# Kernel optimization log

Hardware: AMD Instinct MI355X
Metric: run time of the kernel (lower is better)

The kernel has to match this reference:

```python
import jax, jax.numpy as jnp
import numpy as np

N_ROIS, ROI_DIM, D, H, L, FF, NCLS = 200, 199, 192, 6, 3, 576, 2
EPS = 1e-5

def _ln(x, g, b):
    m = jnp.mean(x, axis=-1, keepdims=True)
    v = jnp.mean((x - m) ** 2, axis=-1, keepdims=True)
    return (x - m) * jax.lax.rsqrt(v + EPS) * g + b

def _gelu(x):
    return jax.nn.gelu(x, approximate=False)

def _mha(q, k, v, Wqkv, bqkv, Wo, bo):
    # q: [B,Q,D], k/v: [B,S,D]; Wqkv: [3,D,D], bqkv: [3,D]
    B, Q, _ = q.shape
    S = k.shape[1]
    Dh = D // H
    qp = (q @ Wqkv[0] + bqkv[0]).reshape(B, Q, H, Dh)
    kp = (k @ Wqkv[1] + bqkv[1]).reshape(B, S, H, Dh)
    vp = (v @ Wqkv[2] + bqkv[2]).reshape(B, S, H, Dh)
    scores = jnp.einsum('bqhd,bkhd->bhqk', qp, kp) / jnp.sqrt(jnp.float32(Dh))
    attn = jax.nn.softmax(scores, axis=-1)
    out = jnp.einsum('bhqk,bkhd->bqhd', attn, vp).reshape(B, Q, D)
    return out @ Wo + bo

def setup_inputs() -> dict:
    key = jax.random.key(0)
    ks = iter(jax.random.split(key, 40))
    r = lambda *s: jax.random.normal(next(ks), s, dtype=jnp.float32) * 0.02
    inp = {
        'x': jax.random.normal(next(ks), (256, N_ROIS * ROI_DIM), dtype=jnp.float32),
        # 200 distinct per-ROI tokenizers, stacked for a single batched GEMM
        'roi_W': r(N_ROIS, ROI_DIM, D), 'roi_b': r(N_ROIS, D),
        'roi_ln_g': jnp.ones((N_ROIS, D), jnp.float32), 'roi_ln_b': jnp.zeros((N_ROIS, D), jnp.float32),
        'pos_emb': r(N_ROIS, D),
        # encoder layers stacked on leading L dim
        'enc_Wqkv': r(L, 3, D, D), 'enc_bqkv': r(L, 3, D),
        'enc_Wo': r(L, D, D), 'enc_bo': r(L, D),
        'enc_ln1_g': jnp.ones((L, D), jnp.float32), 'enc_ln1_b': jnp.zeros((L, D), jnp.float32),
        'enc_W1': r(L, D, FF), 'enc_b1': r(L, FF),
        'enc_W2': r(L, FF, D), 'enc_b2': r(L, D),
        'enc_ln2_g': jnp.ones((L, D), jnp.float32), 'enc_ln2_b': jnp.zeros((L, D), jnp.float32),
        # attention pooling MHA
        'pool_Wqkv': r(3, D, D), 'pool_bqkv': r(3, D),
        'pool_Wo': r(D, D), 'pool_bo': r(D),
        # classifier head
        'cls_ln_g': jnp.ones((D,), jnp.float32), 'cls_ln_b': jnp.zeros((D,), jnp.float32),
        'cls_W1': r(D, D // 2), 'cls_b1': r(D // 2),
        'cls_W2': r(D // 2, D // 4), 'cls_b2': r(D // 4),
        'cls_W3': r(D // 4, NCLS), 'cls_b3': r(NCLS),
    }
    return inp

def reference(x, roi_W, roi_b, roi_ln_g, roi_ln_b, pos_emb,
              enc_Wqkv, enc_bqkv, enc_Wo, enc_bo, enc_ln1_g, enc_ln1_b,
              enc_W1, enc_b1, enc_W2, enc_b2, enc_ln2_g, enc_ln2_b,
              pool_Wqkv, pool_bqkv, pool_Wo, pool_bo,
              cls_ln_g, cls_ln_b, cls_W1, cls_b1, cls_W2, cls_b2, cls_W3, cls_b3):
    B = x.shape[0]
    roi = x.reshape(B, N_ROIS, ROI_DIM)
    # fused per-ROI Linear (200 distinct weights) as one batched GEMM
    tok = jnp.einsum('brf,rfd->brd', roi, roi_W) + roi_b  # [B,200,192]
    tok = _gelu(_ln(tok, roi_ln_g, roi_ln_b))  # dropout = identity (eval)
    tok = tok + pos_emb[None]
    # post-norm transformer encoder (PyTorch default norm_first=False)
    h = tok
    for i in range(L):
        a = _mha(h, h, h, enc_Wqkv[i], enc_bqkv[i], enc_Wo[i], enc_bo[i])
        h = _ln(h + a, enc_ln1_g[i], enc_ln1_b[i])
        f = _gelu(h @ enc_W1[i] + enc_b1[i]) @ enc_W2[i] + enc_b2[i]
        h = _ln(h + f, enc_ln2_g[i], enc_ln2_b[i])
    # MHA pooling: query = mean over ROI tokens
    q = jnp.mean(h, axis=1, keepdims=True)  # [B,1,D]
    pooled = _mha(q, h, h, pool_Wqkv, pool_bqkv, pool_Wo, pool_bo)[:, 0]  # [B,D]
    # classifier
    z = _ln(pooled, cls_ln_g, cls_ln_b)
    z = _gelu(z @ cls_W1 + cls_b1)
    z = _gelu(z @ cls_W2 + cls_b2)
    return z @ cls_W3 + cls_b3
```

## Files before the change

### kernel.cpp

```cpp
#include <hip/hip_runtime.h>
#include <math.h>


typedef unsigned short u16;
typedef unsigned int u32;
typedef __attribute__((ext_vector_type(8))) __bf16 bf16x8;
typedef __attribute__((ext_vector_type(4))) float f32x4;

#define GLL16(gp, lp) __builtin_amdgcn_global_load_lds(                 \
    (const __attribute__((address_space(1))) void*)(gp),                \
    (__attribute__((address_space(3))) void*)(lp), 16, 0, 0)

#define FENCE_VM()   do { asm volatile("s_waitcnt vmcnt(0)" ::: "memory");  \
                          __builtin_amdgcn_sched_barrier(0); } while (0)
#define FENCE_LGKM() do { asm volatile("s_waitcnt lgkmcnt(0)" ::: "memory");\
                          __builtin_amdgcn_sched_barrier(0); } while (0)

__device__ __forceinline__ u16 f2bf(float x) {
    u32 u = __float_as_uint(x);
    u = (u + 0x7FFFu + ((u >> 16) & 1u)) >> 16;
    return (u16)u;
}
__device__ __forceinline__ float bf2f(u16 h) {
    return __uint_as_float(((u32)h) << 16);
}

__device__ __forceinline__ float gelu_exact(float x) {
    return 0.5f * x * (1.0f + erff(x * 0.7071067811865475f));
}

__device__ __forceinline__ float wave_sum(float v) {
#pragma unroll
    for (int o = 32; o > 0; o >>= 1) v += __shfl_xor(v, o, 64);
    return v;
}
__device__ __forceinline__ float wave_max(float v) {
#pragma unroll
    for (int o = 32; o > 0; o >>= 1) v = fmaxf(v, __shfl_xor(v, o, 64));
    return v;
}
__device__ __forceinline__ float row_sum16(float v) {
    v += __shfl_xor(v, 1, 64); v += __shfl_xor(v, 2, 64);
    v += __shfl_xor(v, 4, 64); v += __shfl_xor(v, 8, 64);
    return v;
}

__device__ __forceinline__ f32x4 mfma_bf16(bf16x8 a, bf16x8 b, f32x4 c) {
    return __builtin_amdgcn_mfma_f32_16x16x32_bf16(a, b, c, 0, 0, 0);
}

__global__ void conv_wt(const float* __restrict__ W, u16* __restrict__ oh,
                        int K, int N)
{
    const long z = blockIdx.z;
    const int idx = blockIdx.x * 256 + threadIdx.x;
    if (idx >= K * N) return;
    const int k = idx / N, n = idx - k * N;
    const float x = W[z * K * N + idx];
    oh[z * (long)K * N + (long)n * K + k] = f2bf(x);
}

__global__ void conv_x(const float* __restrict__ x, u16* __restrict__ xh)
{
    const long idx = (long)blockIdx.x * 256 + threadIdx.x;
    if (idx >= 200L * 256 * 224) return;
    const int k = (int)(idx % 224);
    const long t = idx / 224;
    const int m = (int)(t % 256);
    const int z = (int)(t / 256);
    const float v = (k < 199) ? x[(long)m * 39800 + z * 199 + k] : 0.f;
    xh[idx] = f2bf(v);
}

__global__ void conv_roiw(const float* __restrict__ W, u16* __restrict__ oh)
{
    __shared__ float tile[32][33];
    const int z = blockIdx.z;
    const int k0 = blockIdx.x * 32;
    const int n0 = blockIdx.y * 32;
    for (int i = threadIdx.y; i < 32; i += 8) {
        const int k = k0 + i, n = n0 + threadIdx.x;
        tile[i][threadIdx.x] = (k < 199) ? W[((long)z * 199 + k) * 192 + n] : 0.f;
    }
    __syncthreads();
    for (int i = threadIdx.y; i < 32; i += 8) {
        const int n = n0 + i, k = k0 + threadIdx.x;
        const float v = tile[threadIdx.x][i];
        oh[((long)z * 192 + n) * 224 + k] = f2bf(v);
    }
}

template<int EPI>
__global__ __launch_bounds__(256, 3) void gemm_mfma(
    const u16* __restrict__ Ah,
    const u16* __restrict__ Bh,
    const float* __restrict__ bias,
    float* __restrict__ C, u16* __restrict__ Ch,
    u16* __restrict__ Hh, u16* __restrict__ Hl,
    const float* __restrict__ lng, const float* __restrict__ lnb,
    int N, int K)
{
    __shared__ u16 Ash[128][32];
    __shared__ u16 Bsh[192][32];

    const int tid = threadIdx.x;
    const int wave = tid >> 6, lane = tid & 63;
    const int lm = lane & 15, quad = lane >> 4;
    const long m0 = (long)blockIdx.x * 128;
    const int n0 = blockIdx.y * 192;
    const int lrow = lane >> 2;
    const int lch  = (((lane & 3) ^ (lrow & 3)) * 8);
    const int sq   = (quad ^ (lm & 3)) * 8;

    const u16* pA0h = Ah + (m0 + wave * 32 +  0 + lrow) * K + lch;
    const u16* pA1h = Ah + (m0 + wave * 32 + 16 + lrow) * K + lch;
    const u16* pB0h = Bh + (long)(n0 + wave * 48 +  0 + lrow) * K + lch;
    const u16* pB1h = Bh + (long)(n0 + wave * 48 + 16 + lrow) * K + lch;
    const u16* pB2h = Bh + (long)(n0 + wave * 48 + 32 + lrow) * K + lch;

    auto stage = [&](int k0) {
        GLL16(pA0h + k0, &Ash[wave * 32][0]);
        GLL16(pA1h + k0, &Ash[wave * 32 + 16][0]);
        GLL16(pB0h + k0, &Bsh[wave * 48][0]);
        GLL16(pB1h + k0, &Bsh[wave * 48 + 16][0]);
        GLL16(pB2h + k0, &Bsh[wave * 48 + 32][0]);
    };

    f32x4 acc[2][12];
#pragma unroll
    for (int i = 0; i < 2; i++)
#pragma unroll
        for (int j = 0; j < 12; j++)
#pragma unroll
            for (int r = 0; r < 4; r++) acc[i][j][r] = 0.f;

    const int kt = K >> 5;
    stage(0);
    FENCE_VM();
    __syncthreads();

    for (int t = 0; t < kt; t++) {
        bf16x8 afh[2];
#pragma unroll
        for (int mi = 0; mi < 2; mi++)
            afh[mi] = *(const bf16x8*)&Ash[wave * 32 + mi * 16 + lm][sq];
#pragma unroll
        for (int g = 0; g < 4; g++) {
            bf16x8 bfh[3];
#pragma unroll
            for (int j = 0; j < 3; j++)
                bfh[j] = *(const bf16x8*)&Bsh[g * 48 + j * 16 + lm][sq];
#pragma unroll
            for (int mi = 0; mi < 2; mi++)
#pragma unroll
                for (int j = 0; j < 3; j++) {
                    const int ni = g * 3 + j;
                    acc[mi][ni] = mfma_bf16(afh[mi], bfh[j], acc[mi][ni]);
                }
        }
        if (t + 1 < kt) {
            __syncthreads();
            stage((t + 1) << 5);
            FENCE_VM();
            __syncthreads();
        }
    }

    if (EPI == 5) {
        float gv[12], bv2[12], biasv[12];
#pragma unroll
        for (int ni = 0; ni < 12; ni++) {
            const int col = ni * 16 + lm;
            gv[ni] = lng[col]; bv2[ni] = lnb[col]; biasv[ni] = bias[col];
        }
#pragma unroll
        for (int mi = 0; mi < 2; mi++) {
#pragma unroll
            for (int r = 0; r < 4; r++) {
                const long row = m0 + wave * 32 + mi * 16 + quad * 4 + r;
                const long rb = row * 192;
                float vals[12];
                float s = 0.f;
#pragma unroll
                for (int ni = 0; ni < 12; ni++) {
                    const int col = ni * 16 + lm;
                    const float hval = bf2f(Hh[rb + col]) + bf2f(Hl[rb + col]);
                    vals[ni] = acc[mi][ni][r] + biasv[ni] + hval;
                    s += vals[ni];
                }
                const float mean = row_sum16(s) * (1.f / 192.f);
                float ss = 0.f;
#pragma unroll
                for (int ni = 0; ni < 12; ni++) {
                    vals[ni] -= mean;
                    ss += vals[ni] * vals[ni];
                }
                const float var = row_sum16(ss) * (1.f / 192.f);
                const float rsr = 1.f / sqrtf(var + 1e-5f);
#pragma unroll
                for (int ni = 0; ni < 12; ni++) {
                    const int col = ni * 16 + lm;
                    const float y = vals[ni] * rsr * gv[ni] + bv2[ni];
                    const u16 hb = f2bf(y);
                    Hh[rb + col] = hb;
                    Hl[rb + col] = f2bf(y - bf2f(hb));
                }
            }
        }
        return;
    }

#pragma unroll
    for (int mi = 0; mi < 2; mi++) {
        const long rowb = m0 + wave * 32 + mi * 16 + quad * 4;
#pragma unroll
        for (int ni = 0; ni < 12; ni++) {
            const int col = n0 + ni * 16 + lm;
            const float bv = bias[col];
#pragma unroll
            for (int r = 0; r < 4; r++) {
                float v = acc[mi][ni][r] + bv;
                if (EPI == 0) {
                    C[(rowb + r) * N + col] = v;
                } else {
                    if (EPI == 2) v = gelu_exact(v);
                    Ch[(rowb + r) * N + col] = f2bf(v);
                }
            }
        }
    }
}

__global__ __launch_bounds__(256, 3) void tok_mfma(
    const u16* __restrict__ xh,
    const u16* __restrict__ wth,
    const float* __restrict__ roi_b,
    const float* __restrict__ lng, const float* __restrict__ lnb,
    const float* __restrict__ pos,
    u16* __restrict__ hh, u16* __restrict__ hl)
{
    __shared__ u16 Ash[128][32];
    __shared__ u16 Bsh[192][32];

    const int tid = threadIdx.x;
    const int wave = tid >> 6, lane = tid & 63;
    const int lm = lane & 15, quad = lane >> 4;
    const int m0 = blockIdx.x * 128;
    const int z = blockIdx.y;
    const int lrow = lane >> 2;
    const int lch  = (((lane & 3) ^ (lrow & 3)) * 8);
    const int sq   = (quad ^ (lm & 3)) * 8;
    const int K = 224;

    const u16* pA0h = xh + ((long)z * 256 + m0 + wave * 32 +  0 + lrow) * K + lch;
    const u16* pA1h = xh + ((long)z * 256 + m0 + wave * 32 + 16 + lrow) * K + lch;
    const u16* pB0h = wth + ((long)z * 192 + wave * 48 +  0 + lrow) * K + lch;
    const u16* pB1h = wth + ((long)z * 192 + wave * 48 + 16 + lrow) * K + lch;
    const u16* pB2h = wth + ((long)z * 192 + wave * 48 + 32 + lrow) * K + lch;

    auto stage = [&](int k0) {
        GLL16(pA0h + k0, &Ash[wave * 32][0]);
        GLL16(pA1h + k0, &Ash[wave * 32 + 16][0]);
        GLL16(pB0h + k0, &Bsh[wave * 48][0]);
        GLL16(pB1h + k0, &Bsh[wave * 48 + 16][0]);
        GLL16(pB2h + k0, &Bsh[wave * 48 + 32][0]);
    };

    f32x4 acc[2][12];
#pragma unroll
    for (int i = 0; i < 2; i++)
#pragma unroll
        for (int j = 0; j < 12; j++)
#pragma unroll
            for (int r = 0; r < 4; r++) acc[i][j][r] = 0.f;

    stage(0);
    FENCE_VM();
    __syncthreads();
    for (int t = 0; t < 7; t++) {
        bf16x8 afh[2];
#pragma unroll
        for (int mi = 0; mi < 2; mi++)
            afh[mi] = *(const bf16x8*)&Ash[wave * 32 + mi * 16 + lm][sq];
#pragma unroll
        for (int g = 0; g < 4; g++) {
            bf16x8 bfh[3];
#pragma unroll
            for (int j = 0; j < 3; j++)
                bfh[j] = *(const bf16x8*)&Bsh[g * 48 + j * 16 + lm][sq];
#pragma unroll
            for (int mi = 0; mi < 2; mi++)
#pragma unroll
                for (int j = 0; j < 3; j++) {
                    const int ni = g * 3 + j;
                    acc[mi][ni] = mfma_bf16(afh[mi], bfh[j], acc[mi][ni]);
                }
        }
        if (t + 1 < 7) {
            __syncthreads();
            stage((t + 1) << 5);
            FENCE_VM();
            __syncthreads();
        }
    }

    float gv[12], bv2[12], biasv[12], pv[12];
#pragma unroll
    for (int ni = 0; ni < 12; ni++) {
        const int col = ni * 16 + lm;
        gv[ni]    = lng[z * 192 + col];
        bv2[ni]   = lnb[z * 192 + col];
        biasv[ni] = roi_b[z * 192 + col];
        pv[ni]    = pos[z * 192 + col];
    }
#pragma unroll
    for (int mi = 0; mi < 2; mi++) {
#pragma unroll
        for (int r = 0; r < 4; r++) {
            const int brow = m0 + wave * 32 + mi * 16 + quad * 4 + r;
            float vals[12];
            float s = 0.f;
#pragma unroll
            for (int ni = 0; ni < 12; ni++) {
                vals[ni] = acc[mi][ni][r] + biasv[ni];
                s += vals[ni];
            }
            const float mean = row_sum16(s) * (1.f / 192.f);
            float ss = 0.f;
#pragma unroll
            for (int ni = 0; ni < 12; ni++) {
                vals[ni] -= mean;
                ss += vals[ni] * vals[ni];
            }
            const float var = row_sum16(ss) * (1.f / 192.f);
            const float rsr = 1.f / sqrtf(var + 1e-5f);
            const long ob = ((long)brow * 200 + z) * 192;
#pragma unroll
            for (int ni = 0; ni < 12; ni++) {
                const int col = ni * 16 + lm;
                const float y = gelu_exact(vals[ni] * rsr * gv[ni] + bv2[ni]) + pv[ni];
                const u16 hb = f2bf(y);
                hh[ob + col] = hb;
                hl[ob + col] = f2bf(y - bf2f(hb));
            }
        }
    }
}

template<int EPI>
__global__ __launch_bounds__(256) void gemm_kernel(
    const float* __restrict__ A, int lda, long strideA,
    const float* __restrict__ Bw, long strideB,
    const float* __restrict__ bias, long strideBias,
    float* __restrict__ C, int ldc, long strideC,
    int M, int N, int K, int ldb)
{
    __shared__ float As[16][132];
    __shared__ float Bs[16][68];

    const int z = blockIdx.z;
    const float* Ab    = A    + (long)z * strideA;
    const float* Bb    = Bw   + (long)z * strideB;
    const float* biasb = bias + (long)z * strideBias;
    float*       Cb    = C    + (long)z * strideC;

    const int row0 = blockIdx.x * 128;
    const int col0 = blockIdx.y * 64;
    const int tid  = threadIdx.x;
    const int tm = tid >> 4;
    const int tn = tid & 15;

    const int la_m = tid >> 1;
    const int la_k = (tid & 1) * 8;
    const int lb_k = tid >> 4;
    const int lb_n = (tid & 15) * 4;

    const float* bcol = Bb + (col0 + lb_n);
    const float* arow = Ab + (long)(row0 + la_m) * lda;
    const bool vecA = ((lda & 3) == 0) &&
                      ((((unsigned long long)(const void*)arow) & 15ull) == 0ull);

    float acc[8][4];
#pragma unroll
    for (int i = 0; i < 8; i++)
#pragma unroll
        for (int j = 0; j < 4; j++) acc[i][j] = 0.f;

    for (int k0 = 0; k0 < K; k0 += 16) {
        if (vecA && (k0 + 16 <= K)) {
            float4 v0 = *(const float4*)(arow + k0 + la_k);
            float4 v1 = *(const float4*)(arow + k0 + la_k + 4);
            As[la_k + 0][la_m] = v0.x; As[la_k + 1][la_m] = v0.y;
            As[la_k + 2][la_m] = v0.z; As[la_k + 3][la_m] = v0.w;
            As[la_k + 4][la_m] = v1.x; As[la_k + 5][la_m] = v1.y;
            As[la_k + 6][la_m] = v1.z; As[la_k + 7][la_m] = v1.w;
        } else {
#pragma unroll
            for (int i = 0; i < 8; i++) {
                int k = k0 + la_k + i;
                As[la_k + i][la_m] = (k < K) ? arow[k] : 0.f;
            }
        }
        {
            int k = k0 + lb_k;
            float4 v = make_float4(0.f, 0.f, 0.f, 0.f);
            if (k < K) v = *(const float4*)(bcol + (long)k * ldb);
            *(float4*)&Bs[lb_k][lb_n] = v;
        }
        __syncthreads();
#pragma unroll
        for (int kk = 0; kk < 16; kk++) {
            float4 a0 = *(const float4*)&As[kk][tm * 8];
            float4 a1 = *(const float4*)&As[kk][tm * 8 + 4];
            float4 b4 = *(const float4*)&Bs[kk][tn * 4];
            float av[8] = {a0.x, a0.y, a0.z, a0.w, a1.x, a1.y, a1.z, a1.w};
            float bv[4] = {b4.x, b4.y, b4.z, b4.w};
#pragma unroll
            for (int i = 0; i < 8; i++)
#pragma unroll
                for (int j = 0; j < 4; j++) acc[i][j] += av[i] * bv[j];
        }
        __syncthreads();
    }

    const int gcol = col0 + tn * 4;
    float4 bv4 = *(const float4*)(biasb + gcol);
#pragma unroll
    for (int i = 0; i < 8; i++) {
        int grow = row0 + tm * 8 + i;
        float4 o;
        o.x = acc[i][0] + bv4.x; o.y = acc[i][1] + bv4.y;
        o.z = acc[i][2] + bv4.z; o.w = acc[i][3] + bv4.w;
        if (EPI == 1) {
            o.x = gelu_exact(o.x); o.y = gelu_exact(o.y);
            o.z = gelu_exact(o.z); o.w = gelu_exact(o.w);
        }
        *(float4*)(Cb + (long)grow * ldc + gcol) = o;
    }
}

__global__ __launch_bounds__(256, 2) void attn_enc_mfma(
    const u16* __restrict__ qkvh, u16* __restrict__ outh)
{
    __shared__ u16 Ksh[96][40];
    __shared__ u16 Vth[32][104];
    __shared__ u16 Pbuf[4][16][40];

    const int bh = blockIdx.x;
    const int b = bh / 6, h = bh % 6;
    const int tid = threadIdx.x;
    const int wave = tid >> 6, lane = tid & 63;
    const int lm = lane & 15, quad = lane >> 4;
    const int nq = (wave == 0) ? 4 : 3;

    uint4 qh[4];
#pragma unroll
    for (int i = 0; i < 4; i++) {
        if (i < nq) {
            int qt = wave + 4 * i;
            int qrow = qt * 16 + lm; if (qrow > 199) qrow = 199;
            const long off = (long)(b * 200 + qrow) * 576 + h * 32 + quad * 8;
            qh[i] = *(const uint4*)(qkvh + off);
        }
    }

    float mrow[4][4], lrow[4][4];
    f32x4 accO[4][2];
#pragma unroll
    for (int i = 0; i < 4; i++)
#pragma unroll
        for (int r = 0; r < 4; r++) {
            mrow[i][r] = -1e30f; lrow[i][r] = 0.f;
            accO[i][0][r] = 0.f; accO[i][1][r] = 0.f;
        }

    const float scale = 0.17677669529663688f;

#pragma unroll
    for (int ph = 0; ph < 3; ph++) {
        const int base = (ph == 0) ? 0 : (ph == 1) ? 96 : 192;
        const int ntl  = (ph == 2) ? 2 : 6;
        const int nslot = ntl * 16;

        __syncthreads();
        if (wave < 2) {
            const int sub = wave * 64 + lane;
#pragma unroll
            for (int rep = 0; rep < 3; rep++) {
                const int idx = rep * 128 + sub;
                if (idx < nslot * 4) {
                    const int key = idx >> 2, ch = idx & 3;
                    const int gk = base + key;
                    const bool valid = gk < 200;
                    const long roff = (long)(b * 200 + (valid ? gk : 0)) * 576
                                      + h * 32 + 192 + ch * 8;
                    uint4 v = valid ? *(const uint4*)(qkvh + roff)
                                    : make_uint4(0, 0, 0, 0);
                    *(uint4*)(&Ksh[0][0] + key * 40 + ch * 8) = v;
                }
            }
        } else {
            const int sub = (wave - 2) * 64 + lane;
#pragma unroll
            for (int rep = 0; rep < 2; rep++) {
                const int idx = rep * 128 + sub;
                if (idx < nslot * 2) {
                    const int key = idx >> 1, hf = idx & 1;
                    const int gk = base + key;
                    const bool valid = gk < 200;
                    const long roff = (long)(b * 200 + (valid ? gk : 0)) * 576
                                      + h * 32 + 384 + hf * 16;
                    uint4 v0 = valid ? *(const uint4*)(qkvh + roff)
                                     : make_uint4(0, 0, 0, 0);
                    uint4 v1 = valid ? *(const uint4*)(qkvh + roff + 8)
                                     : make_uint4(0, 0, 0, 0);
                    const u16* p0 = (const u16*)&v0;
                    const u16* p1 = (const u16*)&v1;
#pragma unroll
                    for (int j = 0; j < 8; j++) {
                        Vth[hf * 16 + j][key]     = p0[j];
                        Vth[hf * 16 + 8 + j][key] = p1[j];
                    }
                }
            }
        }
        __syncthreads();

#pragma unroll
        for (int i = 0; i < 4; i++) {
            if (i >= nq) continue;
            const bf16x8 qhf = *(const bf16x8*)&qh[i];
            float s[6][4];
#pragma unroll
            for (int ni = 0; ni < 6; ni++) {
                if (ni >= ntl) continue;
                bf16x8 kh8 = *(const bf16x8*)&Ksh[ni * 16 + lm][quad * 8];
                f32x4 c = {0.f, 0.f, 0.f, 0.f};
                c = mfma_bf16(qhf, kh8, c);
                const bool masked = (base + ni * 16 + lm) >= 200;
#pragma unroll
                for (int r = 0; r < 4; r++)
                    s[ni][r] = masked ? -1e30f : c[r] * scale;
            }
            float fac[4];
#pragma unroll
            for (int r = 0; r < 4; r++) {
                float pm = s[0][r];
#pragma unroll
                for (int ni = 1; ni < 6; ni++)
                    if (ni < ntl) pm = fmaxf(pm, s[ni][r]);
                pm = fmaxf(pm, __shfl_xor(pm, 1, 64));
                pm = fmaxf(pm, __shfl_xor(pm, 2, 64));
                pm = fmaxf(pm, __shfl_xor(pm, 4, 64));
                pm = fmaxf(pm, __shfl_xor(pm, 8, 64));
                const float mn = fmaxf(mrow[i][r], pm);
                fac[r] = __expf(mrow[i][r] - mn);
                mrow[i][r] = mn;
                float ps = 0.f;
#pragma unroll
                for (int ni = 0; ni < 6; ni++) {
                    if (ni >= ntl) continue;
                    float e = __expf(s[ni][r] - mn);
                    s[ni][r] = e;
                    ps += e;
                }
                ps += __shfl_xor(ps, 1, 64);
                ps += __shfl_xor(ps, 2, 64);
                ps += __shfl_xor(ps, 4, 64);
                ps += __shfl_xor(ps, 8, 64);
                lrow[i][r] = lrow[i][r] * fac[r] + ps;
                accO[i][0][r] *= fac[r];
                accO[i][1][r] *= fac[r];
            }
#pragma unroll
            for (int ck = 0; ck < 3; ck++) {
                if (ck >= (ntl >> 1)) continue;
                FENCE_LGKM();
#pragma unroll
                for (int tl = 0; tl < 2; tl++) {
#pragma unroll
                    for (int r = 0; r < 4; r++) {
                        Pbuf[wave][quad * 4 + r][tl * 16 + lm] =
                            f2bf(s[2 * ck + tl][r]);
                    }
                }
                FENCE_LGKM();
                const bf16x8 pa = *(const bf16x8*)&Pbuf[wave][lm][quad * 8];
#pragma unroll
                for (int nt = 0; nt < 2; nt++) {
                    bf16x8 vh8 = *(const bf16x8*)&Vth[nt * 16 + lm][ck * 32 + quad * 8];
                    accO[i][nt] = mfma_bf16(pa, vh8, accO[i][nt]);
                }
            }
        }
    }

#pragma unroll
    for (int i = 0; i < 4; i++) {
        if (i >= nq) continue;
        const int qt = wave + 4 * i;
#pragma unroll
        for (int r = 0; r < 4; r++) {
            const int qrow = qt * 16 + quad * 4 + r;
            if (qrow >= 200) continue;
            const float inv = 1.f / lrow[i][r];
            const long ob = (long)(b * 200 + qrow) * 192 + h * 32 + lm;
            outh[ob]      = f2bf(accO[i][0][r] * inv);
            outh[ob + 16] = f2bf(accO[i][1][r] * inv);
        }
    }
}

__global__ __launch_bounds__(192) void mean_tokens_pair(
    const u16* __restrict__ hh, const u16* __restrict__ hl, float* __restrict__ qmean)
{
    const int b = blockIdx.x, d = threadIdx.x;
    float s = 0.f;
    for (int r = 0; r < 200; r++) {
        const long idx = ((long)b * 200 + r) * 192 + d;
        s += bf2f(hh[idx]) + bf2f(hl[idx]);
    }
    qmean[b * 192 + d] = s * (1.f / 200.f);
}

__global__ __launch_bounds__(64) void attn_pool(
    const float* __restrict__ qp, const float* __restrict__ kv,
    float* __restrict__ out)
{
    __shared__ float p[200];
    const int b = blockIdx.x / 6, h = blockIdx.x % 6;
    const int lane = threadIdx.x;

    const float* qrow = qp + b * 192 + h * 32;
    float qr[32];
#pragma unroll
    for (int u = 0; u < 8; u++) {
        float4 t = *(const float4*)(qrow + 4 * u);
        qr[4 * u] = t.x; qr[4 * u + 1] = t.y;
        qr[4 * u + 2] = t.z; qr[4 * u + 3] = t.w;
    }
    const float scale = 0.17677669529663688f;
    const float* kb = kv + (long)(b * 200) * 384 + h * 32;
    float s[4];
    float mymax = -1e30f;
#pragma unroll
    for (int g = 0; g < 4; g++) {
        int j = lane + 64 * g;
        if (j < 200) {
            const float* kr = kb + (long)j * 384;
            float acc = 0.f;
#pragma unroll
            for (int u = 0; u < 8; u++) {
                float4 k4 = *(const float4*)(kr + 4 * u);
                acc += qr[4 * u] * k4.x + qr[4 * u + 1] * k4.y +
                       qr[4 * u + 2] * k4.z + qr[4 * u + 3] * k4.w;
            }
            s[g] = acc * scale;
            mymax = fmaxf(mymax, s[g]);
        } else {
            s[g] = -1e30f;
        }
    }
    float mx = wave_max(mymax);
    float psum = 0.f;
#pragma unroll
    for (int g = 0; g < 4; g++) {
        int j = lane + 64 * g;
        if (j < 200) {
            float e = __expf(s[g] - mx);
            p[j] = e;
            psum += e;
        }
    }
    float tot = wave_sum(psum);
    __syncthreads();
    const int half = lane >> 5, d = lane & 31;
    const float* vb = kv + (long)(b * 200) * 384 + 192 + h * 32 + d;
    float acc = 0.f;
    for (int jj = 0; jj < 100; jj++) {
        int j = half * 100 + jj;
        acc += p[j] * vb[(long)j * 384];
    }
    acc += __shfl_xor(acc, 32, 64);
    acc /= tot;
    if (lane < 32) out[b * 192 + h * 32 + d] = acc;
}

__global__ __launch_bounds__(64) void classifier_kernel(
    const float* __restrict__ pooled,
    const float* __restrict__ g, const float* __restrict__ bt,
    const float* __restrict__ W1, const float* __restrict__ b1,
    const float* __restrict__ W2, const float* __restrict__ b2,
    const float* __restrict__ W3, const float* __restrict__ b3,
    float* __restrict__ out)
{
    __shared__ float z[192];
    __shared__ float z1[96];
    __shared__ float z2[48];
    const int b = blockIdx.x, lane = threadIdx.x;
    const float* pr = pooled + b * 192;
    float x0 = pr[lane], x1 = pr[lane + 64], x2 = pr[lane + 128];
    float m = wave_sum(x0 + x1 + x2) * (1.f / 192.f);
    float d0 = x0 - m, d1 = x1 - m, d2 = x2 - m;
    float v = wave_sum(d0 * d0 + d1 * d1 + d2 * d2) * (1.f / 192.f);
    float rs = 1.f / sqrtf(v + 1e-5f);
    z[lane]       = d0 * rs * g[lane]       + bt[lane];
    z[lane + 64]  = d1 * rs * g[lane + 64]  + bt[lane + 64];
    z[lane + 128] = d2 * rs * g[lane + 128] + bt[lane + 128];
    __syncthreads();
#pragma unroll
    for (int rep = 0; rep < 2; rep++) {
        int j = lane + rep * 64;
        if (j < 96) {
            float a = b1[j];
            for (int k = 0; k < 192; k++) a += z[k] * W1[k * 96 + j];
            z1[j] = gelu_exact(a);
        }
    }
    __syncthreads();
    if (lane < 48) {
        float a = b2[lane];
        for (int k = 0; k < 96; k++) a += z1[k] * W2[k * 48 + lane];
        z2[lane] = gelu_exact(a);
    }
    __syncthreads();
    if (lane < 2) {
        float a = b3[lane];
        for (int k = 0; k < 48; k++) a += z2[k] * W3[k * 2 + lane];
        out[b * 2 + lane] = a;
    }
}

extern "C" void kernel_launch(void* const* d_in, const int* in_sizes, int n_in,
                              void* d_out, int out_size, void* d_ws, size_t ws_size,
                              hipStream_t stream)
{
    (void)in_sizes; (void)n_in; (void)out_size; (void)ws_size;

    const float* x         = (const float*)d_in[0];
    const float* roi_W     = (const float*)d_in[1];
    const float* roi_b     = (const float*)d_in[2];
    const float* roi_ln_g  = (const float*)d_in[3];
    const float* roi_ln_b  = (const float*)d_in[4];
    const float* pos_emb   = (const float*)d_in[5];
    const float* enc_Wqkv  = (const float*)d_in[6];
    const float* enc_bqkv  = (const float*)d_in[7];
    const float* enc_Wo    = (const float*)d_in[8];
    const float* enc_bo    = (const float*)d_in[9];
    const float* enc_ln1_g = (const float*)d_in[10];
    const float* enc_ln1_b = (const float*)d_in[11];
    const float* enc_W1    = (const float*)d_in[12];
    const float* enc_b1    = (const float*)d_in[13];
    const float* enc_W2    = (const float*)d_in[14];
    const float* enc_b2    = (const float*)d_in[15];
    const float* enc_ln2_g = (const float*)d_in[16];
    const float* enc_ln2_b = (const float*)d_in[17];
    const float* pool_Wqkv = (const float*)d_in[18];
    const float* pool_bqkv = (const float*)d_in[19];
    const float* pool_Wo   = (const float*)d_in[20];
    const float* pool_bo   = (const float*)d_in[21];
    const float* cls_ln_g  = (const float*)d_in[22];
    const float* cls_ln_b  = (const float*)d_in[23];
    const float* cls_W1    = (const float*)d_in[24];
    const float* cls_b1    = (const float*)d_in[25];
    const float* cls_W2    = (const float*)d_in[26];
    const float* cls_b2    = (const float*)d_in[27];
    const float* cls_W3    = (const float*)d_in[28];
    const float* cls_b3    = (const float*)d_in[29];

    char* ws = (char*)d_ws;
    u16*   hh    = (u16*)(ws);
    u16*   hl    = (u16*)(ws + 19660800);
    char*  bufA  = ws + 39321600;
    float* bufAf = (float*)bufA;
    u16*   xh    = (u16*)bufA;
    u16*   wth   = (u16*)(bufA + 45875200);
    u16*   qkvh  = (u16*)bufA;
    u16*   ffh   = (u16*)bufA;
    char*  bufB  = ws + 157286400;
    u16*   bBh   = (u16*)bufB;
    float* qmean = (float*)(ws + 196608000);
    float* qp    = qmean + 49152;
    float* pattn = qp + 49152;
    float* pooled= pattn + 49152;
    char*  wts   = ws + 197394432;
    u16* WqkvH = (u16*)(wts);
    u16* Wff1H = (u16*)(wts + 1327104);
    u16* Wff2H = (u16*)(wts + 2654208);
    u16* WwoH  = (u16*)(wts + 3981312);
    u16* WkvH  = (u16*)(wts + 4423680);

    conv_wt<<<dim3(144, 1, 9), 256, 0, stream>>>(enc_Wqkv, WqkvH, 192, 192);
    conv_wt<<<dim3(432, 1, 3), 256, 0, stream>>>(enc_W1, Wff1H, 192, 576);
    conv_wt<<<dim3(432, 1, 3), 256, 0, stream>>>(enc_W2, Wff2H, 576, 192);
    conv_wt<<<dim3(144, 1, 3), 256, 0, stream>>>(enc_Wo, WwoH, 192, 192);
    conv_wt<<<dim3(144, 1, 2), 256, 0, stream>>>(pool_Wqkv + 36864, WkvH, 192, 192);

    conv_x<<<44800, 256, 0, stream>>>(x, xh);
    conv_roiw<<<dim3(7, 6, 200), dim3(32, 8), 0, stream>>>(roi_W, wth);
    tok_mfma<<<dim3(2, 200), 256, 0, stream>>>(
        xh, wth, roi_b, roi_ln_g, roi_ln_b, pos_emb, hh, hl);

    for (int i = 0; i < 3; i++) {
        gemm_mfma<3><<<dim3(400, 3), 256, 0, stream>>>(
            hh, WqkvH + (long)i * 110592,
            enc_bqkv + i * 576, nullptr, qkvh,
            nullptr, nullptr, nullptr, nullptr, 576, 192);
        attn_enc_mfma<<<1536, 256, 0, stream>>>(qkvh, bBh);
        gemm_mfma<5><<<dim3(400, 1), 256, 0, stream>>>(
            bBh, WwoH + (long)i * 36864,
            enc_bo + i * 192, nullptr, nullptr,
            hh, hl, enc_ln1_g + i * 192, enc_ln1_b + i * 192, 192, 192);
        gemm_mfma<2><<<dim3(400, 3), 256, 0, stream>>>(
            hh, Wff1H + (long)i * 110592,
            enc_b1 + i * 576, nullptr, ffh,
            nullptr, nullptr, nullptr, nullptr, 576, 192);
        gemm_mfma<5><<<dim3(400, 1), 256, 0, stream>>>(
            ffh, Wff2H + (long)i * 110592,
            enc_b2 + i * 192, nullptr, nullptr,
            hh, hl, enc_ln2_g + i * 192, enc_ln2_b + i * 192, 192, 576);
    }

    mean_tokens_pair<<<256, 192, 0, stream>>>(hh, hl, qmean);
    gemm_kernel<0><<<dim3(2, 3, 1), 256, 0, stream>>>(
        qmean, 192, 0, pool_Wqkv, 0, pool_bqkv, 0, qp, 192, 0, 256, 192, 192, 192);
    gemm_mfma<0><<<dim3(400, 2), 256, 0, stream>>>(
        hh, WkvH, pool_bqkv + 192,
        bufAf, nullptr,
        nullptr, nullptr, nullptr, nullptr, 384, 192);
    attn_pool<<<1536, 64, 0, stream>>>(qp, bufAf, pattn);
    gemm_kernel<0><<<dim3(2, 3, 1), 256, 0, stream>>>(
        pattn, 192, 0, pool_Wo, 0, pool_bo, 0, pooled, 192, 0, 256, 192, 192, 192);

    classifier_kernel<<<256, 64, 0, stream>>>(
        pooled, cls_ln_g, cls_ln_b,
        cls_W1, cls_b1, cls_W2, cls_b2, cls_W3, cls_b3,
        (float*)d_out);
}
```

Measured before the change: 941.7 us.

## Use 2x2 wave tiling for non-LN GEMMs and double-buffer attention P tiles

The GEMM is split into two kernels. The non-LayerNorm version now arranges its four waves in a 2x2 grid, each computing 64x96, so fewer LDS fragment loads are needed per MFMA. The LN-epilogue version keeps full-row ownership per wave, which the row reduction needs. In encoder attention the P staging buffer is double-buffered per wave, which removes one LDS wait fence per chunk. The cost is higher accumulator register pressure in the 2x2 kernel, which may lower occupancy.

```diff
diff --git a/kernel.cpp b/kernel.cpp
--- a/kernel.cpp
+++ b/kernel.cpp
@@ -91,13 +91,11 @@
 }
 
 template<int EPI>
-__global__ __launch_bounds__(256, 3) void gemm_mfma(
+__global__ __launch_bounds__(256, 3) void gemm_ns(
     const u16* __restrict__ Ah,
     const u16* __restrict__ Bh,
     const float* __restrict__ bias,
     float* __restrict__ C, u16* __restrict__ Ch,
-    u16* __restrict__ Hh, u16* __restrict__ Hl,
-    const float* __restrict__ lng, const float* __restrict__ lnb,
     int N, int K)
 {
     __shared__ u16 Ash[128][32];
@@ -106,6 +104,7 @@
     const int tid = threadIdx.x;
     const int wave = tid >> 6, lane = tid & 63;
     const int lm = lane & 15, quad = lane >> 4;
+    const int wm = wave >> 1, wn = wave & 1;
     const long m0 = (long)blockIdx.x * 128;
     const int n0 = blockIdx.y * 192;
     const int lrow = lane >> 2;
@@ -126,11 +125,11 @@
         GLL16(pB2h + k0, &Bsh[wave * 48 + 32][0]);
     };
 
-    f32x4 acc[2][12];
-#pragma unroll
-    for (int i = 0; i < 2; i++)
-#pragma unroll
-        for (int j = 0; j < 12; j++)
+    f32x4 acc[4][6];
+#pragma unroll
+    for (int i = 0; i < 4; i++)
+#pragma unroll
+        for (int j = 0; j < 6; j++)
 #pragma unroll
             for (int r = 0; r < 4; r++) acc[i][j][r] = 0.f;
 
@@ -140,23 +139,22 @@
     __syncthreads();
 
     for (int t = 0; t < kt; t++) {
-        bf16x8 afh[2];
-#pragma unroll
-        for (int mi = 0; mi < 2; mi++)
-            afh[mi] = *(const bf16x8*)&Ash[wave * 32 + mi * 16 + lm][sq];
-#pragma unroll
-        for (int g = 0; g < 4; g++) {
+        bf16x8 afh[4];
+#pragma unroll
+        for (int mi = 0; mi < 4; mi++)
+            afh[mi] = *(const bf16x8*)&Ash[wm * 64 + mi * 16 + lm][sq];
+#pragma unroll
+        for (int jh = 0; jh < 2; jh++) {
             bf16x8 bfh[3];
 #pragma unroll
             for (int j = 0; j < 3; j++)
-                bfh[j] = *(const bf16x8*)&Bsh[g * 48 + j * 16 + lm][sq];
-#pragma unroll
-            for (int mi = 0; mi < 2; mi++)
-#pragma unroll
-                for (int j = 0; j < 3; j++) {
-                    const int ni = g * 3 + j;
-                    acc[mi][ni] = mfma_bf16(afh[mi], bfh[j], acc[mi][ni]);
-                }
+                bfh[j] = *(const bf16x8*)&Bsh[wn * 96 + (jh * 3 + j) * 16 + lm][sq];
+#pragma unroll
+            for (int mi = 0; mi < 4; mi++)
+#pragma unroll
+                for (int j = 0; j < 3; j++)
+                    acc[mi][jh * 3 + j] =
+                        mfma_bf16(afh[mi], bfh[j], acc[mi][jh * 3 + j]);
         }
         if (t + 1 < kt) {
             __syncthreads();
@@ -166,66 +164,137 @@
         }
     }
 
-    if (EPI == 5) {
-        float gv[12], bv2[12], biasv[12];
-#pragma unroll
-        for (int ni = 0; ni < 12; ni++) {
-            const int col = ni * 16 + lm;
-            gv[ni] = lng[col]; bv2[ni] = lnb[col]; biasv[ni] = bias[col];
-        }
-#pragma unroll
-        for (int mi = 0; mi < 2; mi++) {
+#pragma unroll
+    for (int mi = 0; mi < 4; mi++) {
+        const long rowb = m0 + wm * 64 + mi * 16 + quad * 4;
+#pragma unroll
+        for (int nj = 0; nj < 6; nj++) {
+            const int col = n0 + wn * 96 + nj * 16 + lm;
+            const float bv = bias[col];
 #pragma unroll
             for (int r = 0; r < 4; r++) {
-                const long row = m0 + wave * 32 + mi * 16 + quad * 4 + r;
-                const long rb = row * 192;
-                float vals[12];
-                float s = 0.f;
-#pragma unroll
-                for (int ni = 0; ni < 12; ni++) {
-                    const int col = ni * 16 + lm;
-                    const float hval = bf2f(Hh[rb + col]) + bf2f(Hl[rb + col]);
-                    vals[ni] = acc[mi][ni][r] + biasv[ni] + hval;
-                    s += vals[ni];
-                }
-                const float mean = row_sum16(s) * (1.f / 192.f);
-                float ss = 0.f;
-#pragma unroll
-                for (int ni = 0; ni < 12; ni++) {
-                    vals[ni] -= mean;
-                    ss += vals[ni] * vals[ni];
-                }
-                const float var = row_sum16(ss) * (1.f / 192.f);
-                const float rsr = 1.f / sqrtf(var + 1e-5f);
-#pragma unroll
-                for (int ni = 0; ni < 12; ni++) {
-                    const int col = ni * 16 + lm;
-                    const float y = vals[ni] * rsr * gv[ni] + bv2[ni];
-                    const u16 hb = f2bf(y);
-                    Hh[rb + col] = hb;
-                    Hl[rb + col] = f2bf(y - bf2f(hb));
-                }
-            }
-        }
-        return;
-    }
-
-#pragma unroll
-    for (int mi = 0; mi < 2; mi++) {
-        const long rowb = m0 + wave * 32 + mi * 16 + quad * 4;
-#pragma unroll
-        for (int ni = 0; ni < 12; ni++) {
-            const int col = n0 + ni * 16 + lm;
-            const float bv = bias[col];
-#pragma unroll
-            for (int r = 0; r < 4; r++) {
-                float v = acc[mi][ni][r] + bv;
+                float v = acc[mi][nj][r] + bv;
                 if (EPI == 0) {
                     C[(rowb + r) * N + col] = v;
                 } else {
                     if (EPI == 2) v = gelu_exact(v);
                     Ch[(rowb + r) * N + col] = f2bf(v);
                 }
+            }
+        }
+    }
+}
+
+__global__ __launch_bounds__(256, 3) void gemm_ln(
+    const u16* __restrict__ Ah,
+    const u16* __restrict__ Bh,
+    const float* __restrict__ bias,
+    u16* __restrict__ Hh, u16* __restrict__ Hl,
+    const float* __restrict__ lng, const float* __restrict__ lnb,
+    int K)
+{
+    __shared__ u16 Ash[128][32];
+    __shared__ u16 Bsh[192][32];
+
+    const int tid = threadIdx.x;
+    const int wave = tid >> 6, lane = tid & 63;
+    const int lm = lane & 15, quad = lane >> 4;
+    const long m0 = (long)blockIdx.x * 128;
+    const int lrow = lane >> 2;
+    const int lch  = (((lane & 3) ^ (lrow & 3)) * 8);
+    const int sq   = (quad ^ (lm & 3)) * 8;
+
+    const u16* pA0h = Ah + (m0 + wave * 32 +  0 + lrow) * K + lch;
+    const u16* pA1h = Ah + (m0 + wave * 32 + 16 + lrow) * K + lch;
+    const u16* pB0h = Bh + (long)(wave * 48 +  0 + lrow) * K + lch;
+    const u16* pB1h = Bh + (long)(wave * 48 + 16 + lrow) * K + lch;
+    const u16* pB2h = Bh + (long)(wave * 48 + 32 + lrow) * K + lch;
+
+    auto stage = [&](int k0) {
+        GLL16(pA0h + k0, &Ash[wave * 32][0]);
+        GLL16(pA1h + k0, &Ash[wave * 32 + 16][0]);
+        GLL16(pB0h + k0, &Bsh[wave * 48][0]);
+        GLL16(pB1h + k0, &Bsh[wave * 48 + 16][0]);
+        GLL16(pB2h + k0, &Bsh[wave * 48 + 32][0]);
+    };
+
+    f32x4 acc[2][12];
+#pragma unroll
+    for (int i = 0; i < 2; i++)
+#pragma unroll
+        for (int j = 0; j < 12; j++)
+#pragma unroll
+            for (int r = 0; r < 4; r++) acc[i][j][r] = 0.f;
+
+    const int kt = K >> 5;
+    stage(0);
+    FENCE_VM();
+    __syncthreads();
+
+    for (int t = 0; t < kt; t++) {
+        bf16x8 afh[2];
+#pragma unroll
+        for (int mi = 0; mi < 2; mi++)
+            afh[mi] = *(const bf16x8*)&Ash[wave * 32 + mi * 16 + lm][sq];
+#pragma unroll
+        for (int g = 0; g < 4; g++) {
+            bf16x8 bfh[3];
+#pragma unroll
+            for (int j = 0; j < 3; j++)
+                bfh[j] = *(const bf16x8*)&Bsh[g * 48 + j * 16 + lm][sq];
+#pragma unroll
+            for (int mi = 0; mi < 2; mi++)
+#pragma unroll
+                for (int j = 0; j < 3; j++) {
+                    const int ni = g * 3 + j;
+                    acc[mi][ni] = mfma_bf16(afh[mi], bfh[j], acc[mi][ni]);
+                }
+        }
+        if (t + 1 < kt) {
+            __syncthreads();
+            stage((t + 1) << 5);
+            FENCE_VM();
+            __syncthreads();
+        }
+    }
+
+    float gv[12], bv2[12], biasv[12];
+#pragma unroll
+    for (int ni = 0; ni < 12; ni++) {
+        const int col = ni * 16 + lm;
+        gv[ni] = lng[col]; bv2[ni] = lnb[col]; biasv[ni] = bias[col];
+    }
+#pragma unroll
+    for (int mi = 0; mi < 2; mi++) {
+#pragma unroll
+        for (int r = 0; r < 4; r++) {
+            const long row = m0 + wave * 32 + mi * 16 + quad * 4 + r;
+            const long rb = row * 192;
+            float vals[12];
+            float s = 0.f;
+#pragma unroll
+            for (int ni = 0; ni < 12; ni++) {
+                const int col = ni * 16 + lm;
+                const float hval = bf2f(Hh[rb + col]) + bf2f(Hl[rb + col]);
+                vals[ni] = acc[mi][ni][r] + biasv[ni] + hval;
+                s += vals[ni];
+            }
+            const float mean = row_sum16(s) * (1.f / 192.f);
+            float ss = 0.f;
+#pragma unroll
+            for (int ni = 0; ni < 12; ni++) {
+                vals[ni] -= mean;
+                ss += vals[ni] * vals[ni];
+            }
+            const float var = row_sum16(ss) * (1.f / 192.f);
+            const float rsr = 1.f / sqrtf(var + 1e-5f);
+#pragma unroll
+            for (int ni = 0; ni < 12; ni++) {
+                const int col = ni * 16 + lm;
+                const float y = vals[ni] * rsr * gv[ni] + bv2[ni];
+                const u16 hb = f2bf(y);
+                Hh[rb + col] = hb;
+                Hl[rb + col] = f2bf(y - bf2f(hb));
             }
         }
     }
@@ -444,7 +513,7 @@
 {
     __shared__ u16 Ksh[96][40];
     __shared__ u16 Vth[32][104];
-    __shared__ u16 Pbuf[4][16][40];
+    __shared__ u16 Pbuf[4][2][16][40];
 
     const int bh = blockIdx.x;
     const int b = bh / 6, h = bh % 6;
@@ -475,6 +544,7 @@
         }
 
     const float scale = 0.17677669529663688f;
+    int par = 0;
 
 #pragma unroll
     for (int ph = 0; ph < 3; ph++) {
@@ -575,17 +645,17 @@
 #pragma unroll
             for (int ck = 0; ck < 3; ck++) {
                 if (ck >= (ntl >> 1)) continue;
-                FENCE_LGKM();
+                const int pb = par & 1; par++;
 #pragma unroll
                 for (int tl = 0; tl < 2; tl++) {
 #pragma unroll
                     for (int r = 0; r < 4; r++) {
-                        Pbuf[wave][quad * 4 + r][tl * 16 + lm] =
+                        Pbuf[wave][pb][quad * 4 + r][tl * 16 + lm] =
                             f2bf(s[2 * ck + tl][r]);
                     }
                 }
                 FENCE_LGKM();
-                const bf16x8 pa = *(const bf16x8*)&Pbuf[wave][lm][quad * 8];
+                const bf16x8 pa = *(const bf16x8*)&Pbuf[wave][pb][lm][quad * 8];
 #pragma unroll
                 for (int nt = 0; nt < 2; nt++) {
                     bf16x8 vh8 = *(const bf16x8*)&Vth[nt * 16 + lm][ck * 32 + quad * 8];
@@ -802,32 +872,28 @@
         xh, wth, roi_b, roi_ln_g, roi_ln_b, pos_emb, hh, hl);
 
     for (int i = 0; i < 3; i++) {
-        gemm_mfma<3><<<dim3(400, 3), 256, 0, stream>>>(
+        gemm_ns<3><<<dim3(400, 3), 256, 0, stream>>>(
             hh, WqkvH + (long)i * 110592,
-            enc_bqkv + i * 576, nullptr, qkvh,
-            nullptr, nullptr, nullptr, nullptr, 576, 192);
+            enc_bqkv + i * 576, nullptr, qkvh, 576, 192);
         attn_enc_mfma<<<1536, 256, 0, stream>>>(qkvh, bBh);
-        gemm_mfma<5><<<dim3(400, 1), 256, 0, stream>>>(
+        gemm_ln<<<dim3(400, 1), 256, 0, stream>>>(
             bBh, WwoH + (long)i * 36864,
-            enc_bo + i * 192, nullptr, nullptr,
-            hh, hl, enc_ln1_g + i * 192, enc_ln1_b + i * 192, 192, 192);
-        gemm_mfma<2><<<dim3(400, 3), 256, 0, stream>>>(
+            enc_bo + i * 192,
+            hh, hl, enc_ln1_g + i * 192, enc_ln1_b + i * 192, 192);
+        gemm_ns<2><<<dim3(400, 3), 256, 0, stream>>>(
             hh, Wff1H + (long)i * 110592,
-            enc_b1 + i * 576, nullptr, ffh,
-            nullptr, nullptr, nullptr, nullptr, 576, 192);
-        gemm_mfma<5><<<dim3(400, 1), 256, 0, stream>>>(
+            enc_b1 + i * 576, nullptr, ffh, 576, 192);
+        gemm_ln<<<dim3(400, 1), 256, 0, stream>>>(
             ffh, Wff2H + (long)i * 110592,
-            enc_b2 + i * 192, nullptr, nullptr,
-            hh, hl, enc_ln2_g + i * 192, enc_ln2_b + i * 192, 192, 576);
+            enc_b2 + i * 192,
+            hh, hl, enc_ln2_g + i * 192, enc_ln2_b + i * 192, 576);
     }
 
     mean_tokens_pair<<<256, 192, 0, stream>>>(hh, hl, qmean);
     gemm_kernel<0><<<dim3(2, 3, 1), 256, 0, stream>>>(
         qmean, 192, 0, pool_Wqkv, 0, pool_bqkv, 0, qp, 192, 0, 256, 192, 192, 192);
-    gemm_mfma<0><<<dim3(400, 2), 256, 0, stream>>>(
-        hh, WkvH, pool_bqkv + 192,
-        bufAf, nullptr,
-        nullptr, nullptr, nullptr, nullptr, 384, 192);
+    gemm_ns<0><<<dim3(400, 2), 256, 0, stream>>>(
+        hh, WkvH, pool_bqkv + 192, bufAf, nullptr, 384, 192);
     attn_pool<<<1536, 64, 0, stream>>>(qp, bufAf, pattn);
     gemm_kernel<0><<<dim3(2, 3, 1), 256, 0, stream>>>(
         pattn, 192, 0, pool_Wo, 0, pool_bo, 0, pooled, 192, 0, 256, 192, 192, 192);
```

New measurement: 937.3 us. About the same (-0.5%).
